# Kernel optimization log

Hardware: AMD Instinct MI355X
Metric: run time of the kernel (lower is better)

## Reference

```python
import jax, jax.numpy as jnp
import numpy as np

HIDDEN = 768
N_HEADS = 12
HEAD_DIM = HIDDEN // N_HEADS  # 64
SEQ = 2048
BATCH = 2
ROPE_BASE = 10000.0


def _rope_cos_sin(seq_len, head_dim):
    inv_freq = 1.0 / (ROPE_BASE ** (jnp.arange(0, head_dim, 2, dtype=jnp.float32) / head_dim))
    t = jnp.arange(seq_len, dtype=jnp.float32)
    freqs = jnp.einsum('s,d->sd', t, inv_freq)          # [S, D/2]
    emb = jnp.concatenate([freqs, freqs], axis=-1)      # [S, D]
    return jnp.cos(emb), jnp.sin(emb)


def _rotate_half(x):
    x1, x2 = jnp.split(x, 2, axis=-1)
    return jnp.concatenate([-x2, x1], axis=-1)


def setup_inputs() -> dict:
    key = jax.random.key(0)
    ks = jax.random.split(key, 6)
    scale = 1.0 / np.sqrt(HIDDEN)
    hidden_states = jax.random.normal(ks[0], (BATCH, SEQ, HIDDEN), dtype=jnp.float32)
    wq = jax.random.normal(ks[1], (HIDDEN, HIDDEN), dtype=jnp.float32) * scale
    wk = jax.random.normal(ks[2], (HIDDEN, HIDDEN), dtype=jnp.float32) * scale
    wv = jax.random.normal(ks[3], (HIDDEN, HIDDEN), dtype=jnp.float32) * scale
    wo = jax.random.normal(ks[4], (HIDDEN, HIDDEN), dtype=jnp.float32) * scale
    # additive causal mask: 0 on/below diagonal, large negative above
    causal = jnp.triu(jnp.full((SEQ, SEQ), -1e9, dtype=jnp.float32), k=1)
    attn_mask = causal[None, None, :, :]
    return {"hidden_states": hidden_states, "wq": wq, "wk": wk, "wv": wv,
            "wo": wo, "attn_mask": attn_mask}


def reference(hidden_states, wq, wk, wv, wo, attn_mask):
    B, S, _ = hidden_states.shape
    # projections (nn.Linear: x @ W.T)
    def proj(w):
        y = jnp.einsum('bsh,oh->bso', hidden_states, w)
        return y.reshape(B, S, N_HEADS, HEAD_DIM).transpose(0, 2, 1, 3)  # [B,H,S,D]
    q, k, v = proj(wq), proj(wk), proj(wv)
    cos, sin = _rope_cos_sin(S, HEAD_DIM)  # [S, D]
    cos = cos[None, None, :, :].astype(hidden_states.dtype)
    sin = sin[None, None, :, :].astype(hidden_states.dtype)
    q = q * cos + _rotate_half(q) * sin
    k = k * cos + _rotate_half(k) * sin
    scores = jnp.einsum('bhqd,bhkd->bhqk', q, k) / np.sqrt(HEAD_DIM)
    scores = scores + attn_mask
    probs = jax.nn.softmax(scores.astype(jnp.float32), axis=-1).astype(q.dtype)
    out = jnp.einsum('bhqk,bhkd->bhqd', probs, v)
    out = out.transpose(0, 2, 1, 3).reshape(B, S, HIDDEN)
    return jnp.einsum('bsh,oh->bso', out, wo)
```

## Files before the change

kernel.cpp:

```cpp
#include <hip/hip_runtime.h>

typedef unsigned short u16;
typedef short short8 __attribute__((ext_vector_type(8)));
typedef float f32x4 __attribute__((ext_vector_type(4)));

static_assert(sizeof(short8) == 16, "short8 must be 16B");

__device__ __forceinline__ u16 f2bf(float f) {
  unsigned u = __float_as_uint(f);
  u += 0x7FFFu + ((u >> 16) & 1u);
  return (u16)(u >> 16);
}
__device__ __forceinline__ f32x4 mfma_bf16(short8 a, short8 b, f32x4 c) {
  return __builtin_amdgcn_mfma_f32_16x16x32_bf16(a, b, c, 0, 0, 0);
}
__device__ __forceinline__ void gload_lds16(const void* g, void* l) {
  __builtin_amdgcn_global_load_lds((__attribute__((address_space(1))) void*)g,
                                   (__attribute__((address_space(3))) void*)l, 16, 0, 0);
}
__device__ __forceinline__ float exp2v(float x) {
  float r; asm("v_exp_f32 %0, %1" : "=v"(r) : "v"(x)); return r;
}
__device__ __forceinline__ unsigned cvtpk(float lo, float hi) {
  unsigned r; asm("v_cvt_pk_bf16_f32 %0, %1, %2" : "=v"(r) : "v"(lo), "v"(hi)); return r;
}
__device__ __forceinline__ f32x4 vmax4(f32x4 a, f32x4 b) {
  f32x4 r;
  r[0] = fmaxf(a[0], b[0]); r[1] = fmaxf(a[1], b[1]);
  r[2] = fmaxf(a[2], b[2]); r[3] = fmaxf(a[3], b[3]);
  return r;
}

__global__ __launch_bounds__(256) void cvt_kernel(
    const float* __restrict__ hs, const float* __restrict__ wq, const float* __restrict__ wk,
    const float* __restrict__ wv, const float* __restrict__ wo,
    u16* __restrict__ hbf, u16* __restrict__ wbf) {
  int i = blockIdx.x * 256 + threadIdx.x;
  const float* src; u16* dst; int idx;
  if (i < 786432) {
    src = hs; dst = hbf; idx = i;
  } else {
    int j = i - 786432;
    int seg = j / 147456;
    idx = j - seg * 147456;
    src = (seg == 0) ? wq : (seg == 1) ? wk : (seg == 2) ? wv : wo;
    dst = wbf + seg * 589824;
  }
  float4 v = ((const float4*)src)[idx];
  uint2 r;
  r.x = (unsigned)f2bf(v.x) | ((unsigned)f2bf(v.y) << 16);
  r.y = (unsigned)f2bf(v.z) | ((unsigned)f2bf(v.w) << 16);
  ((uint2*)dst)[idx] = r;
}

template <int MODE>
__global__ __launch_bounds__(256, (MODE == 0) ? 3 : 2) void gemm_bt(
    const u16* __restrict__ A, const u16* __restrict__ Bm,
    u16* __restrict__ qb, u16* __restrict__ kb, u16* __restrict__ vtb,
    float* __restrict__ fout) {
  __shared__ __align__(16) char sm[49152];
  const int K = 768, NK = 12;
  const int t = threadIdx.x;
  const int lane = t & 63;
  const int w = t >> 6;
  const int wr = w >> 1, wc = w & 1;
  const int lrow = lane & 15, lkg = lane >> 4;

  const int l = (MODE == 0) ? ((blockIdx.x & 7) * 144 + (blockIdx.x >> 3))
                            : ((blockIdx.x & 7) * 48 + (blockIdx.x >> 3));
  const int bx = (MODE == 0) ? (l / 18) : (l / 6);
  const int by = (MODE == 0) ? (l % 18) : (l % 6);
  const int arow0 = bx * 64, brow0 = by * 128;

  f32x4 acc[2][4];
  const f32x4 z4 = {0.f, 0.f, 0.f, 0.f};
#pragma unroll
  for (int m = 0; m < 2; ++m)
#pragma unroll
    for (int n = 0; n < 4; ++n) acc[m][n] = z4;

  const int srow = t >> 3;
  const int sslot = t & 7;

  auto STAGE = [&](int ki, int b) {
    char* sA = sm + b * 24576;
    char* sB = sA + 8192;
    const int kt = ki * 64;
#pragma unroll
    for (int it = 0; it < 2; ++it) {
      int r = it * 32 + srow;
      int ls = sslot ^ (r & 7);
      gload_lds16(A + (size_t)(arow0 + r) * K + (kt + ls * 8), sA + it * 4096 + w * 1024);
    }
#pragma unroll
    for (int it = 0; it < 4; ++it) {
      int r = it * 32 + srow;
      int ls = sslot ^ (r & 7);
      gload_lds16(Bm + (size_t)(brow0 + r) * K + (kt + ls * 8), sB + it * 4096 + w * 1024);
    }
  };

  const int g0 = lrow * 128 + ((lkg ^ (lrow & 7)) << 4);
  const int g1 = g0 ^ 64;

  STAGE(0, 0);
  __syncthreads();

  for (int ki = 0; ki < NK; ++ki) {
    const int cur = ki & 1;
    if (ki + 1 < NK) STAGE(ki + 1, cur ^ 1);
    const char* sA = sm + cur * 24576;
    const char* sB = sA + 8192;
#pragma unroll
    for (int kk = 0; kk < 2; ++kk) {
      const int go = kk ? g1 : g0;
      short8 af[2], bfr[4];
#pragma unroll
      for (int m = 0; m < 2; ++m)
        af[m] = *(const short8*)(sA + wr * 4096 + m * 2048 + go);
#pragma unroll
      for (int n = 0; n < 4; ++n)
        bfr[n] = *(const short8*)(sB + wc * 8192 + n * 2048 + go);
#pragma unroll
      for (int m = 0; m < 2; ++m)
#pragma unroll
        for (int n = 0; n < 4; ++n) acc[m][n] = mfma_bf16(af[m], bfr[n], acc[m][n]);
    }
    __syncthreads();
  }

  if (MODE == 1) {
#pragma unroll
    for (int m = 0; m < 2; ++m)
#pragma unroll
      for (int n = 0; n < 4; ++n)
#pragma unroll
        for (int i = 0; i < 4; ++i) {
          int row = arow0 + wr * 32 + m * 16 + lkg * 4 + i;
          int col = brow0 + wc * 64 + n * 16 + lrow;
          fout[(size_t)row * 768 + col] = acc[m][n][i];
        }
  } else {
    const int qsel = brow0 / 768;
    if (qsel < 2) {
      u16* dst = qsel ? kb : qb;
      const float oscale = qsel ? 1.0f : 0.1803368801111244f;
      float fr[2];
      fr[0] = __expf(-0.2878231366242557f * (float)lrow);
      fr[1] = __expf(-0.2878231366242557f * (float)(16 + lrow));
      const int hh = ((brow0 - qsel * 768) >> 6) + wc;
#pragma unroll
      for (int m = 0; m < 2; ++m)
#pragma unroll
        for (int i = 0; i < 4; ++i) {
          int row = arow0 + wr * 32 + m * 16 + lkg * 4 + i;
          int b = row >> 11, s = row & 2047;
          size_t base = ((size_t)(b * 12 + hh) * 2048 + s) * 64;
#pragma unroll
          for (int n2 = 0; n2 < 2; ++n2) {
            float x1 = acc[m][n2][i], x2 = acc[m][n2 + 2][i];
            float th = (float)s * fr[n2];
            float sn, cs;
            __sincosf(th, &sn, &cs);
            dst[base + n2 * 16 + lrow]      = f2bf((x1 * cs - x2 * sn) * oscale);
            dst[base + 32 + n2 * 16 + lrow] = f2bf((x2 * cs + x1 * sn) * oscale);
          }
        }
    } else {
#pragma unroll
      for (int m = 0; m < 2; ++m)
#pragma unroll
        for (int n = 0; n < 4; ++n)
#pragma unroll
          for (int i = 0; i < 4; ++i) {
            int row = arow0 + wr * 32 + m * 16 + lkg * 4 + i;
            int col = brow0 + wc * 64 + n * 16 + lrow;
            int b = row >> 11, s = row & 2047;
            int sc = s & 31;
            int p = ((sc & 12) << 1) | ((sc & 16) >> 2) | (sc & 3);
            int s2 = (s & ~31) | p;
            int oc = col - 1536, h = oc >> 6, d = oc & 63;
            vtb[((size_t)(b * 12 + h) * 64 + d) * 2048 + s2] = f2bf(acc[m][n][i]);
          }
    }
  }
}

__global__ __launch_bounds__(256, 2) void attn_fwd(
    const u16* __restrict__ qg, const u16* __restrict__ kg,
    const u16* __restrict__ vtg, u16* __restrict__ og) {
  __shared__ __align__(16) char sm[65536];
  const int lane = threadIdx.x & 63;
  const int w = threadIdx.x >> 6;
  const int lrow = lane & 15, lkg = lane >> 4;

  const int u = blockIdx.x;
  const int xcd = u & 7, vv = u >> 3;
  const int bh = xcd * 3 + (vv % 3);
  const int qc = 31 - (vv / 3);
  const int qw = qc * 64 + w * 16;
  const int niterS = (qc + 2) >> 1;

  const u16* Q  = qg  + (size_t)bh * (2048 * 64);
  const u16* Kp = kg  + (size_t)bh * (2048 * 64);
  const u16* VT = vtg + (size_t)bh * (64 * 2048);

  short8 qf[2];
#pragma unroll
  for (int h = 0; h < 2; ++h)
    qf[h] = *(const short8*)(Q + (size_t)(qw + lrow) * 64 + h * 32 + lkg * 8);

  const f32x4 z4 = {0.f, 0.f, 0.f, 0.f};
  f32x4 o[4] = {z4, z4, z4, z4};
  float m_ = -1e30f, l_ = 0.f;

  const int a0 = lrow * 128 + ((lkg ^ (lrow & 7)) << 4);
  const int a1 = a0 ^ 64;

  const int s_rl = lane >> 3, s_p = lane & 7;
  const int r0 = w * 16 + s_rl, r1 = r0 + 8;
  const int ls = s_p ^ (r0 & 7);
  const u16* kq0 = Kp + r0 * 64 + ls * 8;
  const u16* kq1 = Kp + r1 * 64 + ls * 8;
  const u16* vq0 = VT + (size_t)r0 * 2048 + ls * 8;
  const u16* vq1 = VT + (size_t)r1 * 2048 + ls * 8;
  const int sdst = w * 2048;

  auto STAGE = [&](int tp, int b) {
    char* sk = sm + b * 32768;
#pragma unroll
    for (int h = 0; h < 2; ++h) {
      const int kvo = tp * 128 + h * 64;
      gload_lds16(kq0 + (size_t)kvo * 64, sk + h * 8192 + sdst);
      gload_lds16(kq1 + (size_t)kvo * 64, sk + h * 8192 + sdst + 1024);
      gload_lds16(vq0 + kvo, sk + 16384 + h * 8192 + sdst);
      gload_lds16(vq1 + kvo, sk + 16384 + h * 8192 + sdst + 1024);
    }
  };

  auto ITER = [&](int t, const char* sk) {
    const char* sv = sk + 16384;
    f32x4 s[2][4];
    __builtin_amdgcn_s_setprio(1);
#pragma unroll
    for (int kb = 0; kb < 4; ++kb) {
#pragma unroll
      for (int h = 0; h < 2; ++h) {
        short8 kf0 = *(const short8*)(sk + h * 8192 + kb * 2048 + a0);
        short8 kf1 = *(const short8*)(sk + h * 8192 + kb * 2048 + a1);
        s[h][kb] = mfma_bf16(kf0, qf[0], z4);
        s[h][kb] = mfma_bf16(kf1, qf[1], s[h][kb]);
      }
    }
    __builtin_amdgcn_s_setprio(0);

    if (t == niterS - 1) {
      int qa = qw + lrow, kv0 = t << 7;
#pragma unroll
      for (int h = 0; h < 2; ++h)
#pragma unroll
        for (int kb = 0; kb < 4; ++kb)
#pragma unroll
          for (int i = 0; i < 4; ++i)
            if (kv0 + h * 64 + kb * 16 + lkg * 4 + i > qa) s[h][kb][i] = -1e30f;
    }

    f32x4 m0 = vmax4(vmax4(s[0][0], s[0][1]), vmax4(s[0][2], s[0][3]));
    f32x4 m1 = vmax4(vmax4(s[1][0], s[1][1]), vmax4(s[1][2], s[1][3]));
    f32x4 m01 = vmax4(m0, m1);
    float mloc = fmaxf(fmaxf(m01[0], m01[1]), fmaxf(m01[2], m01[3]));
    if (__any(mloc > m_ + 8.0f)) {
      float mt = fmaxf(mloc, __shfl_xor(mloc, 16));
      mt = fmaxf(mt, __shfl_xor(mt, 32));
      float mn = fmaxf(m_, mt);
      float sclf = exp2v(m_ - mn);
      m_ = mn;
      l_ *= sclf;
      float sc0 = __shfl(sclf, lkg * 4 + 0);
      float sc1 = __shfl(sclf, lkg * 4 + 1);
      float sc2 = __shfl(sclf, lkg * 4 + 2);
      float sc3 = __shfl(sclf, lkg * 4 + 3);
#pragma unroll
      for (int db = 0; db < 4; ++db) {
        o[db][0] *= sc0; o[db][1] *= sc1; o[db][2] *= sc2; o[db][3] *= sc3;
      }
    }
#pragma unroll
    for (int h = 0; h < 2; ++h)
#pragma unroll
      for (int kb = 0; kb < 4; ++kb)
#pragma unroll
        for (int i = 0; i < 4; ++i) s[h][kb][i] = exp2v(s[h][kb][i] - m_);
    f32x4 st = ((s[0][0] + s[0][1]) + (s[0][2] + s[0][3])) +
               ((s[1][0] + s[1][1]) + (s[1][2] + s[1][3]));
    l_ += (st[0] + st[1]) + (st[2] + st[3]);

    short8 pa[2][2];
#pragma unroll
    for (int h = 0; h < 2; ++h) {
      uint4 p0 = { cvtpk(s[h][0][0], s[h][0][1]), cvtpk(s[h][0][2], s[h][0][3]),
                   cvtpk(s[h][1][0], s[h][1][1]), cvtpk(s[h][1][2], s[h][1][3]) };
      uint4 p1 = { cvtpk(s[h][2][0], s[h][2][1]), cvtpk(s[h][2][2], s[h][2][3]),
                   cvtpk(s[h][3][0], s[h][3][1]), cvtpk(s[h][3][2], s[h][3][3]) };
      pa[h][0] = __builtin_bit_cast(short8, p0);
      pa[h][1] = __builtin_bit_cast(short8, p1);
    }

    __builtin_amdgcn_s_setprio(1);
#pragma unroll
    for (int db = 0; db < 4; ++db) {
#pragma unroll
      for (int h = 0; h < 2; ++h) {
        short8 vf0 = *(const short8*)(sv + h * 8192 + db * 2048 + a0);
        short8 vf1 = *(const short8*)(sv + h * 8192 + db * 2048 + a1);
        o[db] = mfma_bf16(pa[h][0], vf0, o[db]);
        o[db] = mfma_bf16(pa[h][1], vf1, o[db]);
      }
    }
    __builtin_amdgcn_s_setprio(0);
  };

  STAGE(0, 0);
  __syncthreads();

  for (int t = 0; t < niterS; ++t) {
    const int cur = t & 1;
    if (t + 1 < niterS) STAGE(t + 1, cur ^ 1);
    ITER(t, sm + cur * 32768);
    __syncthreads();
  }

  l_ += __shfl_xor(l_, 16);
  l_ += __shfl_xor(l_, 32);
  int b = bh / 12, h = bh - b * 12;
  float nn[4];
  nn[0] = 1.0f / __shfl(l_, lkg * 4 + 0);
  nn[1] = 1.0f / __shfl(l_, lkg * 4 + 1);
  nn[2] = 1.0f / __shfl(l_, lkg * 4 + 2);
  nn[3] = 1.0f / __shfl(l_, lkg * 4 + 3);
#pragma unroll
  for (int i = 0; i < 4; ++i) {
    int qr = qw + lkg * 4 + i;
    u16* orow = og + ((size_t)(b * 2048 + qr)) * 768 + h * 64 + lrow;
    orow[0]  = f2bf(o[0][i] * nn[i]);
    orow[16] = f2bf(o[1][i] * nn[i]);
    orow[32] = f2bf(o[2][i] * nn[i]);
    orow[48] = f2bf(o[3][i] * nn[i]);
  }
}

extern "C" void kernel_launch(void* const* d_in, const int* in_sizes, int n_in,
                              void* d_out, int out_size, void* d_ws, size_t ws_size,
                              hipStream_t stream) {
  const float* hs = (const float*)d_in[0];
  const float* wq = (const float*)d_in[1];
  const float* wk = (const float*)d_in[2];
  const float* wv = (const float*)d_in[3];
  const float* wo = (const float*)d_in[4];
  float* out = (float*)d_out;
  char* ws = (char*)d_ws;

  u16* hbf = (u16*)(ws);
  u16* wbf = (u16*)(ws + 6291456);
  u16* qb  = (u16*)(ws + 11010048);
  u16* kb  = (u16*)(ws + 17301504);
  u16* vtb = (u16*)(ws + 23592960);
  u16* ob  = (u16*)(ws + 29884416);

  cvt_kernel<<<dim3(5376), 256, 0, stream>>>(hs, wq, wk, wv, wo, hbf, wbf);
  gemm_bt<0><<<dim3(1152), 256, 0, stream>>>(hbf, wbf, qb, kb, vtb, nullptr);
  attn_fwd<<<dim3(768), 256, 0, stream>>>(qb, kb, vtb, ob);
  gemm_bt<1><<<dim3(384), 256, 0, stream>>>(ob, wbf + 1769472, nullptr, nullptr, nullptr, out);
}
```

Before: 71.95 us.

## Software-pipeline QK^T of next tile with softmax and split K/V staging

Splits the shared-memory staging into separate double-buffered K and V regions loaded two tiles ahead. The attention loop now computes QK^T for tile t+1 before the softmax and PV of tile t, ping-ponging two score register sets. A single __syncthreads per iteration is replaced by explicit barriers and vmcnt waits. The aim is to overlap MFMA score work with exp/softmax VALU work and hide global-to-LDS latency, at the cost of more live registers, which may hurt occupancy or cause spills at 2 blocks per CU.

After: 72.22 us. Within noise of the previous version (+0.4%).

```diff
diff --git a/kernel.cpp b/kernel.cpp
--- a/kernel.cpp
+++ b/kernel.cpp
@@ -199,7 +199,7 @@
   const int bh = xcd * 3 + (vv % 3);
   const int qc = 31 - (vv / 3);
   const int qw = qc * 64 + w * 16;
-  const int niterS = (qc + 2) >> 1;
+  const int n = (qc + 2) >> 1;
 
   const u16* Q  = qg  + (size_t)bh * (2048 * 64);
   const u16* Kp = kg  + (size_t)bh * (2048 * 64);
@@ -226,21 +226,29 @@
   const u16* vq1 = VT + (size_t)r1 * 2048 + ls * 8;
   const int sdst = w * 2048;
 
-  auto STAGE = [&](int tp, int b) {
-    char* sk = sm + b * 32768;
+  auto STAGE_K = [&](int tp) {
+    char* sk = sm + (tp & 1) * 16384;
 #pragma unroll
     for (int h = 0; h < 2; ++h) {
       const int kvo = tp * 128 + h * 64;
       gload_lds16(kq0 + (size_t)kvo * 64, sk + h * 8192 + sdst);
       gload_lds16(kq1 + (size_t)kvo * 64, sk + h * 8192 + sdst + 1024);
-      gload_lds16(vq0 + kvo, sk + 16384 + h * 8192 + sdst);
-      gload_lds16(vq1 + kvo, sk + 16384 + h * 8192 + sdst + 1024);
     }
   };
-
-  auto ITER = [&](int t, const char* sk) {
-    const char* sv = sk + 16384;
-    f32x4 s[2][4];
+  auto STAGE_V = [&](int tp) {
+    char* sv = sm + 32768 + (tp & 1) * 16384;
+#pragma unroll
+    for (int h = 0; h < 2; ++h) {
+      const int kvo = tp * 128 + h * 64;
+      gload_lds16(vq0 + kvo, sv + h * 8192 + sdst);
+      gload_lds16(vq1 + kvo, sv + h * 8192 + sdst + 1024);
+    }
+  };
+
+  f32x4 s[2][4], s2[2][4];
+
+  auto QKT = [&](int tt, f32x4 (&out)[2][4]) {
+    const char* sk = sm + (tt & 1) * 16384;
     __builtin_amdgcn_s_setprio(1);
 #pragma unroll
     for (int kb = 0; kb < 4; ++kb) {
@@ -248,13 +256,18 @@
       for (int h = 0; h < 2; ++h) {
         short8 kf0 = *(const short8*)(sk + h * 8192 + kb * 2048 + a0);
         short8 kf1 = *(const short8*)(sk + h * 8192 + kb * 2048 + a1);
-        s[h][kb] = mfma_bf16(kf0, qf[0], z4);
-        s[h][kb] = mfma_bf16(kf1, qf[1], s[h][kb]);
+        out[h][kb] = mfma_bf16(kf0, qf[0], z4);
+        out[h][kb] = mfma_bf16(kf1, qf[1], out[h][kb]);
       }
     }
     __builtin_amdgcn_s_setprio(0);
-
-    if (t == niterS - 1) {
+  };
+
+  auto BODY = [&](int t, f32x4 (&scur)[2][4], f32x4 (&snext)[2][4]) {
+    if (t + 2 < n) STAGE_K(t + 2);
+    if (t + 1 < n) QKT(t + 1, snext);
+
+    if (t == n - 1) {
       int qa = qw + lrow, kv0 = t << 7;
 #pragma unroll
       for (int h = 0; h < 2; ++h)
@@ -262,11 +275,11 @@
         for (int kb = 0; kb < 4; ++kb)
 #pragma unroll
           for (int i = 0; i < 4; ++i)
-            if (kv0 + h * 64 + kb * 16 + lkg * 4 + i > qa) s[h][kb][i] = -1e30f;
-    }
-
-    f32x4 m0 = vmax4(vmax4(s[0][0], s[0][1]), vmax4(s[0][2], s[0][3]));
-    f32x4 m1 = vmax4(vmax4(s[1][0], s[1][1]), vmax4(s[1][2], s[1][3]));
+            if (kv0 + h * 64 + kb * 16 + lkg * 4 + i > qa) scur[h][kb][i] = -1e30f;
+    }
+
+    f32x4 m0 = vmax4(vmax4(scur[0][0], scur[0][1]), vmax4(scur[0][2], scur[0][3]));
+    f32x4 m1 = vmax4(vmax4(scur[1][0], scur[1][1]), vmax4(scur[1][2], scur[1][3]));
     f32x4 m01 = vmax4(m0, m1);
     float mloc = fmaxf(fmaxf(m01[0], m01[1]), fmaxf(m01[2], m01[3]));
     if (__any(mloc > m_ + 8.0f)) {
@@ -290,22 +303,23 @@
 #pragma unroll
       for (int kb = 0; kb < 4; ++kb)
 #pragma unroll
-        for (int i = 0; i < 4; ++i) s[h][kb][i] = exp2v(s[h][kb][i] - m_);
-    f32x4 st = ((s[0][0] + s[0][1]) + (s[0][2] + s[0][3])) +
-               ((s[1][0] + s[1][1]) + (s[1][2] + s[1][3]));
+        for (int i = 0; i < 4; ++i) scur[h][kb][i] = exp2v(scur[h][kb][i] - m_);
+    f32x4 st = ((scur[0][0] + scur[0][1]) + (scur[0][2] + scur[0][3])) +
+               ((scur[1][0] + scur[1][1]) + (scur[1][2] + scur[1][3]));
     l_ += (st[0] + st[1]) + (st[2] + st[3]);
 
     short8 pa[2][2];
 #pragma unroll
     for (int h = 0; h < 2; ++h) {
-      uint4 p0 = { cvtpk(s[h][0][0], s[h][0][1]), cvtpk(s[h][0][2], s[h][0][3]),
-                   cvtpk(s[h][1][0], s[h][1][1]), cvtpk(s[h][1][2], s[h][1][3]) };
-      uint4 p1 = { cvtpk(s[h][2][0], s[h][2][1]), cvtpk(s[h][2][2], s[h][2][3]),
-                   cvtpk(s[h][3][0], s[h][3][1]), cvtpk(s[h][3][2], s[h][3][3]) };
+      uint4 p0 = { cvtpk(scur[h][0][0], scur[h][0][1]), cvtpk(scur[h][0][2], scur[h][0][3]),
+                   cvtpk(scur[h][1][0], scur[h][1][1]), cvtpk(scur[h][1][2], scur[h][1][3]) };
+      uint4 p1 = { cvtpk(scur[h][2][0], scur[h][2][1]), cvtpk(scur[h][2][2], scur[h][2][3]),
+                   cvtpk(scur[h][3][0], scur[h][3][1]), cvtpk(scur[h][3][2], scur[h][3][3]) };
       pa[h][0] = __builtin_bit_cast(short8, p0);
       pa[h][1] = __builtin_bit_cast(short8, p1);
     }
 
+    const char* sv = sm + 32768 + (t & 1) * 16384;
     __builtin_amdgcn_s_setprio(1);
 #pragma unroll
     for (int db = 0; db < 4; ++db) {
@@ -318,16 +332,32 @@
       }
     }
     __builtin_amdgcn_s_setprio(0);
+
+    if (t + 1 < n) {
+      __builtin_amdgcn_s_barrier();
+      if (t + 2 < n) {
+        STAGE_V(t + 2);
+        asm volatile("s_waitcnt vmcnt(4)" ::: "memory");
+      } else {
+        asm volatile("s_waitcnt vmcnt(0)" ::: "memory");
+      }
+      __builtin_amdgcn_s_barrier();
+      __builtin_amdgcn_sched_barrier(0);
+    }
   };
 
-  STAGE(0, 0);
-  __syncthreads();
-
-  for (int t = 0; t < niterS; ++t) {
-    const int cur = t & 1;
-    if (t + 1 < niterS) STAGE(t + 1, cur ^ 1);
-    ITER(t, sm + cur * 32768);
-    __syncthreads();
+  STAGE_K(0); STAGE_V(0);
+  if (n > 1) { STAGE_K(1); STAGE_V(1); }
+  asm volatile("s_waitcnt vmcnt(0)" ::: "memory");
+  __builtin_amdgcn_s_barrier();
+  QKT(0, s);
+  __builtin_amdgcn_s_barrier();
+  __builtin_amdgcn_sched_barrier(0);
+
+  int t = 0;
+  while (true) {
+    BODY(t, s, s2); if (++t >= n) break;
+    BODY(t, s2, s); if (++t >= n) break;
   }
 
   l_ += __shfl_xor(l_, 16);
```
